# Kernel tuning notes

Hardware: AMD Instinct MI355X
Metric: run time of the kernel (lower is better)

The kernel has to match this reference:

```python
import jax, jax.numpy as jnp
import numpy as np

V, H, P, L, O = 47, 1024, 4, 3, 47
B, T = 256, 128


def setup_inputs() -> dict:
    key = jax.random.key(0)
    ks = jax.random.split(key, 10)
    s = 1.0 / np.sqrt(H)
    b_ih = jnp.zeros((L, 4 * H), jnp.float32).at[:, H:2 * H].set(1.0)  # forget-gate bias = 1
    return {
        "x": jax.random.randint(ks[0], (B, T), 0, V),
        "properties": jax.random.normal(ks[1], (B, P), jnp.float32),
        "emb": jax.random.normal(ks[2], (V, H), jnp.float32) * s,
        "W_dec": jax.random.normal(ks[3], (O, H), jnp.float32) * s,
        "b_dec": jnp.zeros((O,), jnp.float32),
        "W_ih0": jax.random.normal(ks[4], (4 * H, H + P), jnp.float32) * s,
        "W_ih_rest": jax.random.normal(ks[5], (L - 1, 4 * H, H), jnp.float32) * s,
        "W_hh": jax.random.normal(ks[6], (L, 4 * H, H), jnp.float32) * s,
        "b_ih": b_ih,
        "b_hh": jnp.zeros((L, 4 * H), jnp.float32),
    }


def _lstm_step(x_in, h, c, W_ih, W_hh, b_ih, b_hh):
    # x_in: [B, in_dim]; h, c: [B, H]; gate order i,f,g,o (PyTorch)
    gates = x_in @ W_ih.T + h @ W_hh.T + b_ih + b_hh  # [B, 4H]
    i, f, g, o = jnp.split(gates, 4, axis=-1)
    c_new = jax.nn.sigmoid(f) * c + jax.nn.sigmoid(i) * jnp.tanh(g)
    h_new = jax.nn.sigmoid(o) * jnp.tanh(c_new)
    return h_new, c_new


def reference(x, properties, emb, W_dec, b_dec, W_ih0, W_ih_rest, W_hh, b_ih, b_hh):
    bsz, max_length = x.shape
    h0 = jnp.zeros((L, bsz, H), emb.dtype)
    c0 = jnp.zeros((L, bsz, H), emb.dtype)
    inp0 = emb[jnp.zeros((bsz,), jnp.int32)]  # initial token id 0 -> [B, H]

    def step(carry, _):
        h, c, inp = carry
        x_in = jnp.concatenate([inp, properties], axis=-1)  # [B, H+P]
        hs, cs = [], []
        for l in range(L):
            W_ih_l = W_ih0 if l == 0 else W_ih_rest[l - 1]
            h_l, c_l = _lstm_step(x_in, h[l], c[l], W_ih_l, W_hh[l], b_ih[l], b_hh[l])
            hs.append(h_l); cs.append(c_l)
            x_in = h_l
        logits = x_in @ W_dec.T + b_dec  # [B, O]
        nxt = jnp.argmax(logits, axis=-1)  # greedy decode
        new_carry = (jnp.stack(hs), jnp.stack(cs), emb[nxt])
        return new_carry, logits

    (h, c, _), logits_seq = jax.lax.scan(step, (h0, c0, inp0), None, length=max_length)
    outputs = jnp.transpose(logits_seq, (1, 0, 2))  # [B, T, O]
    return outputs, h, c
```

## Files before the change

kernel.cpp:

```cpp
#include <hip/hip_runtime.h>
#include <hip/hip_bf16.h>
#include <cstdint>
#include <cstddef>


#define BB 256
#define TT 128
#define OO 47

typedef __attribute__((ext_vector_type(8))) _Float16 f16x8;
typedef __attribute__((ext_vector_type(4))) float f32x4;

#define CBUF_B   0u
#define HF32_B   3145728u
#define BCOMB_B  9437184u
#define EHI_B    9486336u
#define ELO_B    10027008u
#define HS_B     10567680u
#define W_B      16859136u
#define WS_NEEDED 118046720u

#define BARRIER() asm volatile("s_barrier" ::: "memory")
#define WAITV(n)  asm volatile("s_waitcnt vmcnt(" #n ")" ::: "memory")
#define WAITLGKM0() asm volatile("s_waitcnt lgkmcnt(0)" ::: "memory")

__device__ __forceinline__ float fsig(float x) {
  return 1.0f / (1.0f + exp2f(-1.4426950408889634f * x));
}
__device__ __forceinline__ float ftanhf(float x) {
  float e = exp2f(2.8853900817779268f * x);
  return 1.0f - 2.0f / (e + 1.0f);
}
__device__ __forceinline__ unsigned short f16b(_Float16 h) {
  union { _Float16 f; unsigned short u; } c; c.f = h; return c.u;
}
__device__ __forceinline__ void gld16(const void* g, void* l) {
  __builtin_amdgcn_global_load_lds(
      (const __attribute__((address_space(1))) unsigned int*)g,
      (__attribute__((address_space(3))) unsigned int*)l, 16, 0, 0);
}
__device__ __forceinline__ size_t slab_addr(int grp, int NCH, int k, int r) {
  return ((size_t)grp * NCH + (k >> 5)) * 512 + ((k >> 4) & 1) * 256 +
         ((k >> 3) & 1) * 128 + r * 8 + (k & 7);
}

__global__ void k_zero(float* p, int n) {
  int i = blockIdx.x * blockDim.x + threadIdx.x;
  int stride = gridDim.x * blockDim.x;
  for (; i < n; i += stride) p[i] = 0.0f;
}

__global__ void k_binit(float* bc, const float* __restrict__ bih,
                        const float* __restrict__ bhh) {
  int i = blockIdx.x * blockDim.x + threadIdx.x;
  if (i < 12288) bc[i] = bih[i] + bhh[i];
}

__global__ void k_prepw(const float* __restrict__ src, unsigned short* dhi,
                        unsigned short* dlo, int K, int NCH) {
  const int nrow = blockIdx.x;
  const int ngrp = nrow >> 4, rr = nrow & 15;
  const float* s = src + (size_t)nrow * K;
  for (int k = threadIdx.x; k < NCH * 32; k += blockDim.x) {
    float val = (k < K) ? s[k] : 0.0f;
    _Float16 h16 = (_Float16)val;
    _Float16 l16 = (_Float16)((val - (float)h16) * 2048.0f);
    size_t a = slab_addr(ngrp, NCH, k, rr);
    dhi[a] = f16b(h16);
    dlo[a] = f16b(l16);
  }
}

__global__ void k_einit(unsigned short* ehi, unsigned short* elo,
                        const float* __restrict__ emb,
                        const float* __restrict__ props) {
  const int b = blockIdx.x;
  for (int j = threadIdx.x; j < 1056; j += blockDim.x) {
    float val = (j < 1024) ? emb[j] : (j < 1028 ? props[b * 4 + (j - 1024)] : 0.0f);
    _Float16 h16 = (_Float16)val;
    _Float16 l16 = (_Float16)((val - (float)h16) * 2048.0f);
    size_t a = slab_addr(b >> 4, 33, j, b & 15);
    ehi[a] = f16b(h16);
    elo[a] = f16b(l16);
  }
}

__global__ __launch_bounds__(512, 4) void k_layer(
    const char* __restrict__ xhi, const char* __restrict__ xlo, int NCHX,
    const char* __restrict__ hhi, const char* __restrict__ hlo,
    const char* __restrict__ wxhi, const char* __restrict__ wxlo,
    const char* __restrict__ whhi, const char* __restrict__ whlo,
    const float* __restrict__ bcomb, float* __restrict__ cbuf,
    float* __restrict__ hdstf, unsigned short* __restrict__ hshi,
    unsigned short* __restrict__ hslo) {
  __shared__ char LBUF[65536];
  const int tid = threadIdx.x;
  const int lane = tid & 63, wid = tid >> 6;
  const int sw = ((blockIdx.x & 7) << 5) + (blockIdx.x >> 3);
  const int mt = sw & 3, nt = sw >> 2;
  const int m0 = mt << 6, h0c = nt << 4;
  const int nst = (NCHX > 32) ? NCHX : 32;

  const int sIsB = wid >> 2, sHalfW = (wid >> 1) & 1, sPrec = wid & 1;
  const int sNch = sHalfW ? 32 : NCHX;
  const char* sbase[4];
  {
    const char* t0;
    if (!sIsB) t0 = sHalfW ? (sPrec ? hlo : hhi) : (sPrec ? xlo : xhi);
    else       t0 = sHalfW ? (sPrec ? whlo : whhi) : (sPrec ? wxlo : wxhi);
#pragma unroll
    for (int i = 0; i < 4; ++i) {
      int grp = sIsB ? (i * 64 + nt) : (mt * 4 + i);
      sbase[i] = t0 + (size_t)grp * sNch * 1024 + (size_t)lane * 16;
    }
  }
  const int ldsoff0 = (sIsB << 14) + (sHalfW << 13) + (sPrec << 12);
  auto stage = [&](int s, int bufbase) {
    char* ldst = LBUF + bufbase + ldsoff0;
    const size_t so = (size_t)s * 1024;
#pragma unroll
    for (int i = 0; i < 4; ++i) gld16(sbase[i] + so, ldst + i * 1024);
  };

  const int wHalf = wid >> 2, q = wid & 3;
  const int mb = (q >> 1) << 1, nbb = (q & 1) << 1;
  const int waveNst = wHalf ? 32 : NCHX;

  f32x4 accH[4], accL[4];
#pragma unroll
  for (int i = 0; i < 4; ++i) {
    accH[i] = f32x4{0.f, 0.f, 0.f, 0.f};
    accL[i] = f32x4{0.f, 0.f, 0.f, 0.f};
  }

  stage(0, 0);
  stage(1, 32768);

  for (int s = 0; s < nst; ++s) {
    const int bufb = (s & 1) << 15;
    if (s + 1 < sNch) { WAITV(4); }
    else              { WAITV(0); }
    BARRIER();

    if (s < waveNst) {
      const char* A0 = LBUF + bufb + (wHalf << 13);
      const char* B0 = LBUF + bufb + 16384 + (wHalf << 13);
      f16x8 ah[2], al[2], bh[2], bl[2];
#pragma unroll
      for (int r = 0; r < 2; ++r) {
        ah[r] = *(const f16x8*)(A0 + ((mb + r) << 10) + (lane << 4));
        al[r] = *(const f16x8*)(A0 + 4096 + ((mb + r) << 10) + (lane << 4));
      }
#pragma unroll
      for (int c = 0; c < 2; ++c) {
        bh[c] = *(const f16x8*)(B0 + ((nbb + c) << 10) + (lane << 4));
        bl[c] = *(const f16x8*)(B0 + 4096 + ((nbb + c) << 10) + (lane << 4));
      }
      __builtin_amdgcn_s_setprio(1);
#pragma unroll
      for (int r = 0; r < 2; ++r)
#pragma unroll
        for (int c = 0; c < 2; ++c) {
          int ix = r * 2 + c;
          accH[ix] = __builtin_amdgcn_mfma_f32_16x16x32_f16(ah[r], bh[c], accH[ix], 0, 0, 0);
          accL[ix] = __builtin_amdgcn_mfma_f32_16x16x32_f16(al[r], bh[c], accL[ix], 0, 0, 0);
          accL[ix] = __builtin_amdgcn_mfma_f32_16x16x32_f16(ah[r], bl[c], accL[ix], 0, 0, 0);
        }
      __builtin_amdgcn_s_setprio(0);
    }

    WAITLGKM0();
    BARRIER();
    if (s + 2 < sNch) stage(s + 2, bufb);
  }

  BARRIER();
  float* GH = (float*)LBUF;
  float* GL = GH + 64 * 68;
  const int mrow0 = ((q >> 1) << 5) + ((lane >> 4) << 2);
  const int ncol0 = ((q & 1) << 5) + (lane & 15);
  if (wHalf == 0) {
#pragma unroll
    for (int r = 0; r < 2; ++r)
#pragma unroll
      for (int c = 0; c < 2; ++c) {
        f32x4 aH = accH[r * 2 + c], aL = accL[r * 2 + c];
        int mr = mrow0 + r * 16, nc = ncol0 + c * 16;
#pragma unroll
        for (int i = 0; i < 4; ++i) {
          GH[(mr + i) * 68 + nc] = aH[i];
          GL[(mr + i) * 68 + nc] = aL[i];
        }
      }
  }
  __syncthreads();
  if (wHalf == 1) {
#pragma unroll
    for (int r = 0; r < 2; ++r)
#pragma unroll
      for (int c = 0; c < 2; ++c) {
        f32x4 aH = accH[r * 2 + c], aL = accL[r * 2 + c];
        int mr = mrow0 + r * 16, nc = ncol0 + c * 16;
#pragma unroll
        for (int i = 0; i < 4; ++i) {
          GH[(mr + i) * 68 + nc] += aH[i];
          GL[(mr + i) * 68 + nc] += aL[i];
        }
      }
  }
  __syncthreads();

  const float LSC = 1.0f / 2048.0f;
#pragma unroll
  for (int e = 0; e < 2; ++e) {
    int ci = tid * 2 + e;
    int bl_ = ci >> 4, hh = ci & 15;
    int b = m0 + bl_, hcol = h0c + hh;
    float xi = GH[bl_ * 68 + hh]      + GL[bl_ * 68 + hh]      * LSC + bcomb[hcol];
    float xf = GH[bl_ * 68 + 16 + hh] + GL[bl_ * 68 + 16 + hh] * LSC + bcomb[1024 + hcol];
    float xg = GH[bl_ * 68 + 32 + hh] + GL[bl_ * 68 + 32 + hh] * LSC + bcomb[2048 + hcol];
    float xo = GH[bl_ * 68 + 48 + hh] + GL[bl_ * 68 + 48 + hh] * LSC + bcomb[3072 + hcol];
    size_t cidx = (size_t)b * 1024 + hcol;
    float cn = fsig(xf) * cbuf[cidx] + fsig(xi) * ftanhf(xg);
    float hn = fsig(xo) * ftanhf(cn);
    cbuf[cidx] = cn;
    hdstf[cidx] = hn;
    _Float16 h16 = (_Float16)hn;
    _Float16 l16 = (_Float16)((hn - (float)h16) * 2048.0f);
    size_t sa = slab_addr(b >> 4, 32, hcol, b & 15);
    hshi[sa] = f16b(h16);
    hslo[sa] = f16b(l16);
  }
}

__global__ __launch_bounds__(256) void k_decode(
    const float* __restrict__ h2, const float* __restrict__ Wdec,
    const float* __restrict__ bdec, const float* __restrict__ emb,
    float* __restrict__ out, unsigned short* __restrict__ ehi,
    unsigned short* __restrict__ elo, int t) {
  __shared__ float P[4][64];
  __shared__ int tokS;
  const int b = blockIdx.x;
  const int w = threadIdx.x >> 6, lane = threadIdx.x & 63;
  const float* hrow = h2 + (size_t)b * 1024 + w * 256;
  float part = 0.f;
  if (lane < OO) {
    const float* wrow = Wdec + (size_t)lane * 1024 + w * 256;
    float p0 = 0.f, p1 = 0.f, p2 = 0.f, p3 = 0.f;
    for (int k = 0; k < 256; k += 16) {
      float4 w0 = *(const float4*)(wrow + k);      float4 h0v = *(const float4*)(hrow + k);
      float4 w1 = *(const float4*)(wrow + k + 4);  float4 h1v = *(const float4*)(hrow + k + 4);
      float4 w2 = *(const float4*)(wrow + k + 8);  float4 h2v = *(const float4*)(hrow + k + 8);
      float4 w3 = *(const float4*)(wrow + k + 12); float4 h3v = *(const float4*)(hrow + k + 12);
      p0 += w0.x * h0v.x + w0.y * h0v.y + w0.z * h0v.z + w0.w * h0v.w;
      p1 += w1.x * h1v.x + w1.y * h1v.y + w1.z * h1v.z + w1.w * h1v.w;
      p2 += w2.x * h2v.x + w2.y * h2v.y + w2.z * h2v.z + w2.w * h2v.w;
      p3 += w3.x * h3v.x + w3.y * h3v.y + w3.z * h3v.z + w3.w * h3v.w;
    }
    part = (p0 + p1) + (p2 + p3);
  }
  P[w][lane] = part;
  __syncthreads();
  if (w == 0) {
    float logit = -3.0e38f;
    if (lane < OO)
      logit = P[0][lane] + P[1][lane] + P[2][lane] + P[3][lane] + bdec[lane];
    float vv = logit;
    int idx = (lane < OO) ? lane : 1000;
#pragma unroll
    for (int m = 1; m < 64; m <<= 1) {
      float v2 = __shfl_xor(vv, m, 64);
      int i2 = __shfl_xor(idx, m, 64);
      if (v2 > vv || (v2 == vv && i2 < idx)) { vv = v2; idx = i2; }
    }
    if (lane < OO) out[(size_t)b * (TT * OO) + t * OO + lane] = logit;
    if (lane == 0) tokS = idx;
  }
  __syncthreads();
  if (t < TT - 1) {
    const float* erow = emb + (size_t)tokS * 1024;
    float4 ev = ((const float4*)erow)[threadIdx.x];
    float vals[4] = {ev.x, ev.y, ev.z, ev.w};
#pragma unroll
    for (int r = 0; r < 4; ++r) {
      int j = threadIdx.x * 4 + r;
      _Float16 h16 = (_Float16)vals[r];
      _Float16 l16 = (_Float16)((vals[r] - (float)h16) * 2048.0f);
      size_t a = slab_addr(b >> 4, 33, j, b & 15);
      ehi[a] = f16b(h16);
      elo[a] = f16b(l16);
    }
  }
}

__global__ void k_final(const float* __restrict__ hf, const float* __restrict__ cb,
                        float* __restrict__ out) {
  int i = blockIdx.x * blockDim.x + threadIdx.x;
  int stride = gridDim.x * blockDim.x;
  const int HBASE = BB * TT * OO;
  for (; i < 2 * 786432; i += stride) {
    if (i < 786432) {
      int l = i >> 18, r = i & 262143;
      out[HBASE + i] = hf[(size_t)(l * 2 + 0) * 262144 + r];
    } else {
      int j = i - 786432;
      out[HBASE + 786432 + j] = cb[j];
    }
  }
}

#define O_EBUF  0
#define O_HPB   270336
#define O_CBUF  1843200
#define O_BCOMB 2629632
#define O_WSN   2641920
#define O_HP(l, p) (O_HPB + ((l) * 2 + (p)) * 262144)

__global__ void k_initO(float* ws, const float* __restrict__ props,
                        const float* __restrict__ emb,
                        const float* __restrict__ bih,
                        const float* __restrict__ bhh) {
  int i = blockIdx.x * blockDim.x + threadIdx.x;
  if (i < 270336) {
    int b = i / 1056, j = i % 1056;
    float v = 0.0f;
    if (j < 1024) v = emb[j];
    else if (j < 1028) v = props[b * 4 + (j - 1024)];
    ws[O_EBUF + i] = v;
  } else if (i < 270336 + 12288) {
    int j = i - 270336;
    ws[O_BCOMB + j] = bih[j] + bhh[j];
  }
}

__global__ __launch_bounds__(512, 2) void k_layerO(
    const float* __restrict__ xsrc, int xs, int Kx, int nst0,
    const float* __restrict__ hsrc,
    const float* __restrict__ Wx, int wxs,
    const float* __restrict__ Wh,
    const float* __restrict__ bcomb, float* __restrict__ cbuf,
    float* __restrict__ hdst) {
  __shared__ char LBUF[65536];
  const int tid = threadIdx.x;
  const int lane = tid & 63, wid = tid >> 6;
  const int sw = ((blockIdx.x & 7) << 5) + (blockIdx.x >> 3);
  const int mt = sw & 3, nt = sw >> 2;
  const int m0 = mt << 6, h0c = nt << 4;
  const int nstMax = (nst0 > 32) ? nst0 : 32;
  const int tile = tid >> 7;
  const int tt = tid & 127;
  const int srow = tt >> 1;
  const int kseg = (tt & 1) << 4;
  const int isB = tile >> 1, sHalf = tile & 1;
  const int myNst = sHalf ? 32 : nst0;
  const float* grow;
  int KactB = 0x7fffffff;
  if (!isB) {
    grow = sHalf ? (hsrc + (size_t)(m0 + srow) * 1024)
                 : (xsrc + (size_t)(m0 + srow) * xs);
  } else {
    int nrow = ((srow >> 4) << 10) + h0c + (srow & 15);
    grow = sHalf ? (Wh + (size_t)nrow * 1024) : (Wx + (size_t)nrow * wxs);
    KactB = sHalf ? 1024 : Kx;
  }
  const int wbase = ((srow >> 4) << 10) + ((tt & 1) << 9) + ((srow & 15) << 4);
  const int ssec = (isB << 14) + (sHalf << 13);
  const int wHalf = wid >> 2, q = wid & 3;
  const int mb = (q >> 1) << 1, nbb = (q & 1) << 1;
  const int waveNst = wHalf ? 32 : nst0;
  const int secAr = (wHalf << 13);
  const int secBr = 16384 + (wHalf << 13);
  f32x4 accH[4], accL[4];
#pragma unroll
  for (int i = 0; i < 4; ++i) {
    accH[i] = f32x4{0.f, 0.f, 0.f, 0.f};
    accL[i] = f32x4{0.f, 0.f, 0.f, 0.f};
  }
  float4 v[4];
  auto load_regs = [&](int s) {
    const int kl = (s << 5) + kseg;
    const float4* p = (const float4*)(grow + kl);
#pragma unroll
    for (int qq = 0; qq < 4; ++qq) {
      int kk = kl + qq * 4;
      if (kk < KactB) v[qq] = p[qq];
      else v[qq] = float4{0.f, 0.f, 0.f, 0.f};
    }
  };
  auto cvt_write = [&](int buf) {
    char* base = LBUF + buf * 32768 + ssec + wbase;
#pragma unroll
    for (int g = 0; g < 2; ++g) {
      float fs[8] = {v[2*g].x, v[2*g].y, v[2*g].z, v[2*g].w,
                     v[2*g+1].x, v[2*g+1].y, v[2*g+1].z, v[2*g+1].w};
      f16x8 hvv, lvv;
#pragma unroll
      for (int j = 0; j < 8; ++j) {
        _Float16 h16 = (_Float16)fs[j];
        lvv[j] = (_Float16)((fs[j] - (float)h16) * 2048.0f);
        hvv[j] = h16;
      }
      *(f16x8*)(base + g * 256) = hvv;
      *(f16x8*)(base + g * 256 + 4096) = lvv;
    }
  };
  load_regs(0);
  cvt_write(0);
  __syncthreads();
  for (int s = 0; s < nstMax; ++s) {
    const int cur = s & 1, nxt = cur ^ 1;
    const bool doStage = (s + 1 < myNst);
    if (doStage) load_regs(s + 1);
    if (s < waveNst) {
      const char* A0 = LBUF + cur * 32768 + secAr;
      const char* B0 = LBUF + cur * 32768 + secBr;
      f16x8 ah[2], al[2], bh[2], bl[2];
#pragma unroll
      for (int r = 0; r < 2; ++r) {
        ah[r] = *(const f16x8*)(A0 + ((mb + r) << 10) + (lane << 4));
        al[r] = *(const f16x8*)(A0 + 4096 + ((mb + r) << 10) + (lane << 4));
      }
#pragma unroll
      for (int c = 0; c < 2; ++c) {
        bh[c] = *(const f16x8*)(B0 + ((nbb + c) << 10) + (lane << 4));
        bl[c] = *(const f16x8*)(B0 + 4096 + ((nbb + c) << 10) + (lane << 4));
      }
#pragma unroll
      for (int r = 0; r < 2; ++r)
#pragma unroll
        for (int c = 0; c < 2; ++c) {
          int ix = r * 2 + c;
          accH[ix] = __builtin_amdgcn_mfma_f32_16x16x32_f16(ah[r], bh[c], accH[ix], 0, 0, 0);
          accL[ix] = __builtin_amdgcn_mfma_f32_16x16x32_f16(al[r], bh[c], accL[ix], 0, 0, 0);
          accL[ix] = __builtin_amdgcn_mfma_f32_16x16x32_f16(ah[r], bl[c], accL[ix], 0, 0, 0);
        }
    }
    if (doStage) cvt_write(nxt);
    __syncthreads();
  }
  float* GH = (float*)LBUF;
  float* GL = GH + 64 * 68;
  const int mrow0 = ((q >> 1) << 5) + ((lane >> 4) << 2);
  const int ncol0 = ((q & 1) << 5) + (lane & 15);
  if (wHalf == 0) {
#pragma unroll
    for (int r = 0; r < 2; ++r)
#pragma unroll
      for (int c = 0; c < 2; ++c) {
        f32x4 aHh = accH[r * 2 + c], aLl = accL[r * 2 + c];
        int mr = mrow0 + r * 16, nc = ncol0 + c * 16;
#pragma unroll
        for (int i = 0; i < 4; ++i) { GH[(mr + i) * 68 + nc] = aHh[i]; GL[(mr + i) * 68 + nc] = aLl[i]; }
      }
  }
  __syncthreads();
  if (wHalf == 1) {
#pragma unroll
    for (int r = 0; r < 2; ++r)
#pragma unroll
      for (int c = 0; c < 2; ++c) {
        f32x4 aHh = accH[r * 2 + c], aLl = accL[r * 2 + c];
        int mr = mrow0 + r * 16, nc = ncol0 + c * 16;
#pragma unroll
        for (int i = 0; i < 4; ++i) { GH[(mr + i) * 68 + nc] += aHh[i]; GL[(mr + i) * 68 + nc] += aLl[i]; }
      }
  }
  __syncthreads();
  const float LSC = 1.0f / 2048.0f;
#pragma unroll
  for (int e = 0; e < 2; ++e) {
    int ci = tid * 2 + e;
    int bl_ = ci >> 4, hh = ci & 15;
    int b = m0 + bl_, hcol = h0c + hh;
    float xi = GH[bl_ * 68 + hh]      + GL[bl_ * 68 + hh]      * LSC + bcomb[hcol];
    float xf = GH[bl_ * 68 + 16 + hh] + GL[bl_ * 68 + 16 + hh] * LSC + bcomb[1024 + hcol];
    float xg = GH[bl_ * 68 + 32 + hh] + GL[bl_ * 68 + 32 + hh] * LSC + bcomb[2048 + hcol];
    float xo = GH[bl_ * 68 + 48 + hh] + GL[bl_ * 68 + 48 + hh] * LSC + bcomb[3072 + hcol];
    size_t cidx = (size_t)b * 1024 + hcol;
    float cn = fsig(xf) * cbuf[cidx] + fsig(xi) * ftanhf(xg);
    float hn = fsig(xo) * ftanhf(cn);
    cbuf[cidx] = cn;
    hdst[cidx] = hn;
  }
}

__global__ __launch_bounds__(64) void k_decodeO(
    const float* __restrict__ h2, const float* __restrict__ Wdec,
    const float* __restrict__ bdec, const float* __restrict__ emb,
    float* __restrict__ out, float* __restrict__ ebuf, int t) {
  const int b = blockIdx.x, lane = threadIdx.x;
  const float* hrow = h2 + (size_t)b * 1024;
  float logit = 0.f;
  if (lane < OO) {
    const float* wrow = Wdec + (size_t)lane * 1024;
    float p0 = 0.f, p1 = 0.f, p2 = 0.f, p3 = 0.f;
    for (int k = 0; k < 1024; k += 16) {
      float4 w0 = *(const float4*)(wrow + k);      float4 h0v = *(const float4*)(hrow + k);
      float4 w1 = *(const float4*)(wrow + k + 4);  float4 h1v = *(const float4*)(hrow + k + 4);
      float4 w2 = *(const float4*)(wrow + k + 8);  float4 h2v = *(const float4*)(hrow + k + 8);
      float4 w3 = *(const float4*)(wrow + k + 12); float4 h3v = *(const float4*)(hrow + k + 12);
      p0 += w0.x * h0v.x + w0.y * h0v.y + w0.z * h0v.z + w0.w * h0v.w;
      p1 += w1.x * h1v.x + w1.y * h1v.y + w1.z * h1v.z + w1.w * h1v.w;
      p2 += w2.x * h2v.x + w2.y * h2v.y + w2.z * h2v.z + w2.w * h2v.w;
      p3 += w3.x * h3v.x + w3.y * h3v.y + w3.z * h3v.z + w3.w * h3v.w;
    }
    logit = ((p0 + p1) + (p2 + p3)) + bdec[lane];
  }
  float vv = (lane < OO) ? logit : -3.0e38f;
  int idx = (lane < OO) ? lane : 1000;
#pragma unroll
  for (int m = 1; m < 64; m <<= 1) {
    float v2 = __shfl_xor(vv, m, 64);
    int i2 = __shfl_xor(idx, m, 64);
    if (v2 > vv || (v2 == vv && i2 < idx)) { vv = v2; idx = i2; }
  }
  if (lane < OO) out[(size_t)b * (TT * OO) + t * OO + lane] = logit;
  if (t < TT - 1) {
    const float* erow = emb + (size_t)idx * 1024;
#pragma unroll
    for (int i = 0; i < 16; ++i) {
      int h = i * 64 + lane;
      ebuf[(size_t)b * 1056 + h] = erow[h];
    }
  }
}

__global__ void k_finalO(const float* __restrict__ ws, float* __restrict__ out) {
  int i = blockIdx.x * blockDim.x + threadIdx.x;
  int stride = gridDim.x * blockDim.x;
  const int HBASE = BB * TT * OO;
  for (; i < 2 * 786432; i += stride) {
    if (i < 786432) {
      int l = i >> 18, r = i & 262143;
      out[HBASE + i] = ws[O_HP(l, 0) + r];
    } else {
      int j = i - 786432;
      out[HBASE + 786432 + j] = ws[O_CBUF + j];
    }
  }
}

extern "C" void kernel_launch(void* const* d_in, const int* in_sizes, int n_in,
                              void* d_out, int out_size, void* d_ws, size_t ws_size,
                              hipStream_t stream) {
  const float* props = (const float*)d_in[1];
  const float* emb   = (const float*)d_in[2];
  const float* Wdec  = (const float*)d_in[3];
  const float* bdec  = (const float*)d_in[4];
  const float* Wih0  = (const float*)d_in[5];
  const float* Wihr  = (const float*)d_in[6];
  const float* Whh   = (const float*)d_in[7];
  const float* bih   = (const float*)d_in[8];
  const float* bhh   = (const float*)d_in[9];
  float* out = (float*)d_out;

  if (ws_size >= (size_t)WS_NEEDED) {
    char* base = (char*)d_ws;
    float* cb = (float*)(base + CBUF_B);
    float* hf = (float*)(base + HF32_B);
    float* bc = (float*)(base + BCOMB_B);
    unsigned short* Ehi = (unsigned short*)(base + EHI_B);
    unsigned short* Elo = (unsigned short*)(base + ELO_B);
    auto HS = [&](int l, int p, int prec) {
      return (unsigned short*)(base + HS_B + (size_t)((l * 2 + p) * 2 + prec) * 524288u);
    };
    unsigned short* Wp[12];
    {
      size_t off = W_B;
      Wp[0] = (unsigned short*)(base + off); off += 8650752u;
      Wp[1] = (unsigned short*)(base + off); off += 8650752u;
      for (int i = 2; i < 12; ++i) { Wp[i] = (unsigned short*)(base + off); off += 8388608u; }
    }

    k_zero<<<2048, 256, 0, stream>>>((float*)base, 2359296);
    k_zero<<<2048, 256, 0, stream>>>((float*)(base + HS_B), 1572864);
    k_binit<<<48, 256, 0, stream>>>(bc, bih, bhh);
    k_einit<<<256, 256, 0, stream>>>(Ehi, Elo, emb, props);
    k_prepw<<<4096, 256, 0, stream>>>(Wih0, Wp[0], Wp[1], 1028, 33);
    k_prepw<<<4096, 256, 0, stream>>>(Whh,                           Wp[2], Wp[3], 1024, 32);
    k_prepw<<<4096, 256, 0, stream>>>(Wihr,                          Wp[4], Wp[5], 1024, 32);
    k_prepw<<<4096, 256, 0, stream>>>(Whh + (size_t)4096 * 1024,     Wp[6], Wp[7], 1024, 32);
    k_prepw<<<4096, 256, 0, stream>>>(Wihr + (size_t)4096 * 1024,    Wp[8], Wp[9], 1024, 32);
    k_prepw<<<4096, 256, 0, stream>>>(Whh + (size_t)2 * 4096 * 1024, Wp[10], Wp[11], 1024, 32);

    for (int t = 0; t < TT; ++t) {
      const int p = t & 1, pn = p ^ 1;
      k_layer<<<256, 512, 0, stream>>>(
          (const char*)Ehi, (const char*)Elo, 33,
          (const char*)HS(0, p, 0), (const char*)HS(0, p, 1),
          (const char*)Wp[0], (const char*)Wp[1],
          (const char*)Wp[2], (const char*)Wp[3],
          bc, cb, hf + (size_t)(0 * 2 + pn) * 262144,
          HS(0, pn, 0), HS(0, pn, 1));
      k_layer<<<256, 512, 0, stream>>>(
          (const char*)HS(0, pn, 0), (const char*)HS(0, pn, 1), 32,
          (const char*)HS(1, p, 0), (const char*)HS(1, p, 1),
          (const char*)Wp[4], (const char*)Wp[5],
          (const char*)Wp[6], (const char*)Wp[7],
          bc + 4096, cb + 262144, hf + (size_t)(1 * 2 + pn) * 262144,
          HS(1, pn, 0), HS(1, pn, 1));
      k_layer<<<256, 512, 0, stream>>>(
          (const char*)HS(1, pn, 0), (const char*)HS(1, pn, 1), 32,
          (const char*)HS(2, p, 0), (const char*)HS(2, p, 1),
          (const char*)Wp[8], (const char*)Wp[9],
          (const char*)Wp[10], (const char*)Wp[11],
          bc + 8192, cb + 524288, hf + (size_t)(2 * 2 + pn) * 262144,
          HS(2, pn, 0), HS(2, pn, 1));
      k_decode<<<256, 256, 0, stream>>>(hf + (size_t)(2 * 2 + pn) * 262144,
                                        Wdec, bdec, emb, out, Ehi, Elo, t);
    }
    k_final<<<2048, 256, 0, stream>>>(hf, cb, out);
  } else {
    float* ws = (float*)d_ws;
    float* E  = ws + O_EBUF;
    float* cb = ws + O_CBUF;
    float* bc = ws + O_BCOMB;
    k_zero<<<2048, 256, 0, stream>>>(ws, O_WSN);
    k_initO<<<1104, 256, 0, stream>>>(ws, props, emb, bih, bhh);
    for (int t = 0; t < TT; ++t) {
      const int p = t & 1;
      k_layerO<<<256, 512, 0, stream>>>(E, 1056, 1028, 33, ws + O_HP(0, p),
                                        Wih0, 1028, Whh, bc, cb, ws + O_HP(0, p ^ 1));
      k_layerO<<<256, 512, 0, stream>>>(ws + O_HP(0, p ^ 1), 1024, 1024, 32,
                                        ws + O_HP(1, p), Wihr, 1024,
                                        Whh + (size_t)4096 * 1024,
                                        bc + 4096, cb + 262144, ws + O_HP(1, p ^ 1));
      k_layerO<<<256, 512, 0, stream>>>(ws + O_HP(1, p ^ 1), 1024, 1024, 32,
                                        ws + O_HP(2, p),
                                        Wihr + (size_t)4096 * 1024, 1024,
                                        Whh + (size_t)2 * 4096 * 1024,
                                        bc + 8192, cb + 524288, ws + O_HP(2, p ^ 1));
      k_decodeO<<<256, 64, 0, stream>>>(ws + O_HP(2, p ^ 1), Wdec, bdec, emb, out, E, t);
    }
    k_finalO<<<2048, 256, 0, stream>>>(ws, out);
  }
}
```

Measured before the change: 10.33 ms.

## Fuse per-step layer and decode launches into one persistent kernel with grid barriers

Replaces the 512 per-timestep kernel launches (three layers plus decode, 128 steps) with a single persistent kernel of 256 blocks. Blocks synchronise through a hierarchical atomic grid barrier: a counter per group of eight, then a global generation counter. This removes launch overhead and the implicit inter-kernel gaps. The cost is spin-wait barrier latency and a requirement that all 256 blocks be co-resident, since otherwise the barrier deadlocks. Decode now spreads across 8 waves instead of 4.

```diff
diff --git a/kernel.cpp b/kernel.cpp
--- a/kernel.cpp
+++ b/kernel.cpp
@@ -18,7 +18,8 @@
 #define ELO_B    10027008u
 #define HS_B     10567680u
 #define W_B      16859136u
-#define WS_NEEDED 118046720u
+#define BAR_B    118046720u
+#define WS_NEEDED 118047360u
 
 #define BARRIER() asm volatile("s_barrier" ::: "memory")
 #define WAITV(n)  asm volatile("s_waitcnt vmcnt(" #n ")" ::: "memory")
@@ -51,9 +52,10 @@
 }
 
 __global__ void k_binit(float* bc, const float* __restrict__ bih,
-                        const float* __restrict__ bhh) {
+                        const float* __restrict__ bhh, unsigned* bar) {
   int i = blockIdx.x * blockDim.x + threadIdx.x;
   if (i < 12288) bc[i] = bih[i] + bhh[i];
+  if (i < 160) bar[i] = 0u;
 }
 
 __global__ void k_prepw(const float* __restrict__ src, unsigned short* dhi,
@@ -85,210 +87,277 @@
   }
 }
 
-__global__ __launch_bounds__(512, 4) void k_layer(
-    const char* __restrict__ xhi, const char* __restrict__ xlo, int NCHX,
-    const char* __restrict__ hhi, const char* __restrict__ hlo,
-    const char* __restrict__ wxhi, const char* __restrict__ wxlo,
-    const char* __restrict__ whhi, const char* __restrict__ whlo,
-    const float* __restrict__ bcomb, float* __restrict__ cbuf,
-    float* __restrict__ hdstf, unsigned short* __restrict__ hshi,
-    unsigned short* __restrict__ hslo) {
+__device__ __forceinline__ void gbar(unsigned* bar, int bid) {
+  __syncthreads();
+  if (threadIdx.x == 0) {
+    unsigned* gen  = bar + 144;
+    unsigned* gcnt = bar + 128;
+    unsigned* myg  = bar + ((bid & 7) << 4);
+    unsigned g = __hip_atomic_load(gen, __ATOMIC_RELAXED, __HIP_MEMORY_SCOPE_AGENT);
+    unsigned o = __hip_atomic_fetch_add(myg, 1u, __ATOMIC_ACQ_REL, __HIP_MEMORY_SCOPE_AGENT);
+    if (o == 31u) {
+      __hip_atomic_store(myg, 0u, __ATOMIC_RELAXED, __HIP_MEMORY_SCOPE_AGENT);
+      unsigned og = __hip_atomic_fetch_add(gcnt, 1u, __ATOMIC_ACQ_REL, __HIP_MEMORY_SCOPE_AGENT);
+      if (og == 7u) {
+        __hip_atomic_store(gcnt, 0u, __ATOMIC_RELAXED, __HIP_MEMORY_SCOPE_AGENT);
+        __hip_atomic_store(gen, g + 1u, __ATOMIC_RELEASE, __HIP_MEMORY_SCOPE_AGENT);
+      }
+    }
+    while (__hip_atomic_load(gen, __ATOMIC_RELAXED, __HIP_MEMORY_SCOPE_AGENT) == g) {
+      asm volatile("s_sleep 2");
+    }
+    (void)__hip_atomic_load(gen, __ATOMIC_ACQUIRE, __HIP_MEMORY_SCOPE_AGENT);
+  }
+  __syncthreads();
+  if ((threadIdx.x & 63) == 0)
+    (void)__hip_atomic_load(bar + 144, __ATOMIC_ACQUIRE, __HIP_MEMORY_SCOPE_AGENT);
+}
+
+__global__ __launch_bounds__(512, 4) void k_mega(
+    char* __restrict__ base, const float* __restrict__ Wdec,
+    const float* __restrict__ bdec, const float* __restrict__ emb,
+    float* __restrict__ out) {
   __shared__ char LBUF[65536];
   const int tid = threadIdx.x;
   const int lane = tid & 63, wid = tid >> 6;
-  const int sw = ((blockIdx.x & 7) << 5) + (blockIdx.x >> 3);
+  const int bid = blockIdx.x;
+  const int sw = ((bid & 7) << 5) + (bid >> 3);
   const int mt = sw & 3, nt = sw >> 2;
   const int m0 = mt << 6, h0c = nt << 4;
-  const int nst = (NCHX > 32) ? NCHX : 32;
+
+  unsigned* bar = (unsigned*)(base + BAR_B);
+  float* cbufA = (float*)(base + CBUF_B);
+  float* hfA   = (float*)(base + HF32_B);
+  float* bcA   = (float*)(base + BCOMB_B);
+
+  const unsigned wOff[12] = {
+    16859136u, 25509888u, 34160640u, 42549248u, 50937856u, 59326464u,
+    67715072u, 76103680u, 84492288u, 92880896u, 101269504u, 109658112u};
 
   const int sIsB = wid >> 2, sHalfW = (wid >> 1) & 1, sPrec = wid & 1;
-  const int sNch = sHalfW ? 32 : NCHX;
-  const char* sbase[4];
-  {
-    const char* t0;
-    if (!sIsB) t0 = sHalfW ? (sPrec ? hlo : hhi) : (sPrec ? xlo : xhi);
-    else       t0 = sHalfW ? (sPrec ? whlo : whhi) : (sPrec ? wxlo : wxhi);
-#pragma unroll
-    for (int i = 0; i < 4; ++i) {
-      int grp = sIsB ? (i * 64 + nt) : (mt * 4 + i);
-      sbase[i] = t0 + (size_t)grp * sNch * 1024 + (size_t)lane * 16;
-    }
-  }
   const int ldsoff0 = (sIsB << 14) + (sHalfW << 13) + (sPrec << 12);
-  auto stage = [&](int s, int bufbase) {
-    char* ldst = LBUF + bufbase + ldsoff0;
-    const size_t so = (size_t)s * 1024;
-#pragma unroll
-    for (int i = 0; i < 4; ++i) gld16(sbase[i] + so, ldst + i * 1024);
-  };
-
   const int wHalf = wid >> 2, q = wid & 3;
   const int mb = (q >> 1) << 1, nbb = (q & 1) << 1;
-  const int waveNst = wHalf ? 32 : NCHX;
-
-  f32x4 accH[4], accL[4];
-#pragma unroll
-  for (int i = 0; i < 4; ++i) {
-    accH[i] = f32x4{0.f, 0.f, 0.f, 0.f};
-    accL[i] = f32x4{0.f, 0.f, 0.f, 0.f};
-  }
-
-  stage(0, 0);
-  stage(1, 32768);
-
-  for (int s = 0; s < nst; ++s) {
-    const int bufb = (s & 1) << 15;
-    if (s + 1 < sNch) { WAITV(4); }
-    else              { WAITV(0); }
-    BARRIER();
-
-    if (s < waveNst) {
-      const char* A0 = LBUF + bufb + (wHalf << 13);
-      const char* B0 = LBUF + bufb + 16384 + (wHalf << 13);
-      f16x8 ah[2], al[2], bh[2], bl[2];
-#pragma unroll
-      for (int r = 0; r < 2; ++r) {
-        ah[r] = *(const f16x8*)(A0 + ((mb + r) << 10) + (lane << 4));
-        al[r] = *(const f16x8*)(A0 + 4096 + ((mb + r) << 10) + (lane << 4));
-      }
-#pragma unroll
-      for (int c = 0; c < 2; ++c) {
-        bh[c] = *(const f16x8*)(B0 + ((nbb + c) << 10) + (lane << 4));
-        bl[c] = *(const f16x8*)(B0 + 4096 + ((nbb + c) << 10) + (lane << 4));
-      }
-      __builtin_amdgcn_s_setprio(1);
-#pragma unroll
-      for (int r = 0; r < 2; ++r)
-#pragma unroll
-        for (int c = 0; c < 2; ++c) {
-          int ix = r * 2 + c;
-          accH[ix] = __builtin_amdgcn_mfma_f32_16x16x32_f16(ah[r], bh[c], accH[ix], 0, 0, 0);
-          accL[ix] = __builtin_amdgcn_mfma_f32_16x16x32_f16(al[r], bh[c], accL[ix], 0, 0, 0);
-          accL[ix] = __builtin_amdgcn_mfma_f32_16x16x32_f16(ah[r], bl[c], accL[ix], 0, 0, 0);
-        }
-      __builtin_amdgcn_s_setprio(0);
-    }
-
-    WAITLGKM0();
-    BARRIER();
-    if (s + 2 < sNch) stage(s + 2, bufb);
-  }
-
-  BARRIER();
-  float* GH = (float*)LBUF;
-  float* GL = GH + 64 * 68;
   const int mrow0 = ((q >> 1) << 5) + ((lane >> 4) << 2);
   const int ncol0 = ((q & 1) << 5) + (lane & 15);
-  if (wHalf == 0) {
-#pragma unroll
-    for (int r = 0; r < 2; ++r)
-#pragma unroll
-      for (int c = 0; c < 2; ++c) {
-        f32x4 aH = accH[r * 2 + c], aL = accL[r * 2 + c];
-        int mr = mrow0 + r * 16, nc = ncol0 + c * 16;
-#pragma unroll
-        for (int i = 0; i < 4; ++i) {
-          GH[(mr + i) * 68 + nc] = aH[i];
-          GL[(mr + i) * 68 + nc] = aL[i];
+  const float LSC = 1.0f / 2048.0f;
+
+  for (int t = 0; t < TT; ++t) {
+    const int p = t & 1, pn = p ^ 1;
+
+    for (int l = 0; l < 3; ++l) {
+      const char *xhi, *xlo;
+      int NCHX;
+      if (l == 0) { xhi = base + EHI_B; xlo = base + ELO_B; NCHX = 33; }
+      else {
+        xhi = base + HS_B + (size_t)(((l - 1) * 2 + pn) * 2 + 0) * 524288u;
+        xlo = base + HS_B + (size_t)(((l - 1) * 2 + pn) * 2 + 1) * 524288u;
+        NCHX = 32;
+      }
+      const char* hhi = base + HS_B + (size_t)((l * 2 + p) * 2 + 0) * 524288u;
+      const char* hlo = base + HS_B + (size_t)((l * 2 + p) * 2 + 1) * 524288u;
+      const int wbase4 = (l == 0) ? 0 : (l == 1 ? 4 : 8);
+      const char* wxhi = base + wOff[wbase4 + 0];
+      const char* wxlo = base + wOff[wbase4 + 1];
+      const char* whhi = base + wOff[wbase4 + 2];
+      const char* whlo = base + wOff[wbase4 + 3];
+      const float* bcomb = bcA + l * 4096;
+      float* cbuf  = cbufA + (size_t)l * 262144;
+      float* hdstf = hfA + (size_t)(l * 2 + pn) * 262144;
+      unsigned short* hshi = (unsigned short*)(base + HS_B + (size_t)((l * 2 + pn) * 2 + 0) * 524288u);
+      unsigned short* hslo = (unsigned short*)(base + HS_B + (size_t)((l * 2 + pn) * 2 + 1) * 524288u);
+
+      const int nst = (NCHX > 32) ? NCHX : 32;
+      const int sNch = sHalfW ? 32 : NCHX;
+      const int waveNst = wHalf ? 32 : NCHX;
+
+      const char* sb0;
+      {
+        const char* t0;
+        if (!sIsB) t0 = sHalfW ? (sPrec ? hlo : hhi) : (sPrec ? xlo : xhi);
+        else       t0 = sHalfW ? (sPrec ? whlo : whhi) : (sPrec ? wxlo : wxhi);
+        sb0 = t0 + (size_t)lane * 16;
+      }
+      const char* sb[4];
+#pragma unroll
+      for (int i = 0; i < 4; ++i) {
+        int grp = sIsB ? (i * 64 + nt) : (mt * 4 + i);
+        sb[i] = sb0 + (size_t)grp * sNch * 1024;
+      }
+      auto stage = [&](int s, int bufbase) {
+        char* ldst = LBUF + bufbase + ldsoff0;
+        const size_t so = (size_t)s * 1024;
+#pragma unroll
+        for (int i = 0; i < 4; ++i) gld16(sb[i] + so, ldst + i * 1024);
+      };
+
+      f32x4 accH[4], accL[4];
+#pragma unroll
+      for (int i = 0; i < 4; ++i) {
+        accH[i] = f32x4{0.f, 0.f, 0.f, 0.f};
+        accL[i] = f32x4{0.f, 0.f, 0.f, 0.f};
+      }
+
+      stage(0, 0);
+      stage(1, 32768);
+
+      for (int s = 0; s < nst; ++s) {
+        const int bufb = (s & 1) << 15;
+        if (s + 1 < sNch) { WAITV(4); }
+        else              { WAITV(0); }
+        BARRIER();
+
+        if (s < waveNst) {
+          const char* A0 = LBUF + bufb + (wHalf << 13);
+          const char* B0 = LBUF + bufb + 16384 + (wHalf << 13);
+          f16x8 ah[2], al[2], bh[2], bl[2];
+#pragma unroll
+          for (int r = 0; r < 2; ++r) {
+            ah[r] = *(const f16x8*)(A0 + ((mb + r) << 10) + (lane << 4));
+            al[r] = *(const f16x8*)(A0 + 4096 + ((mb + r) << 10) + (lane << 4));
+          }
+#pragma unroll
+          for (int c = 0; c < 2; ++c) {
+            bh[c] = *(const f16x8*)(B0 + ((nbb + c) << 10) + (lane << 4));
+            bl[c] = *(const f16x8*)(B0 + 4096 + ((nbb + c) << 10) + (lane << 4));
+          }
+          __builtin_amdgcn_s_setprio(1);
+#pragma unroll
+          for (int r = 0; r < 2; ++r)
+#pragma unroll
+            for (int c = 0; c < 2; ++c) {
+              int ix = r * 2 + c;
+              accH[ix] = __builtin_amdgcn_mfma_f32_16x16x32_f16(ah[r], bh[c], accH[ix], 0, 0, 0);
+              accL[ix] = __builtin_amdgcn_mfma_f32_16x16x32_f16(al[r], bh[c], accL[ix], 0, 0, 0);
+              accL[ix] = __builtin_amdgcn_mfma_f32_16x16x32_f16(ah[r], bl[c], accL[ix], 0, 0, 0);
+            }
+          __builtin_amdgcn_s_setprio(0);
         }
-      }
-  }
-  __syncthreads();
-  if (wHalf == 1) {
-#pragma unroll
-    for (int r = 0; r < 2; ++r)
-#pragma unroll
-      for (int c = 0; c < 2; ++c) {
-        f32x4 aH = accH[r * 2 + c], aL = accL[r * 2 + c];
-        int mr = mrow0 + r * 16, nc = ncol0 + c * 16;
-#pragma unroll
-        for (int i = 0; i < 4; ++i) {
-          GH[(mr + i) * 68 + nc] += aH[i];
-          GL[(mr + i) * 68 + nc] += aL[i];
+
+        WAITLGKM0();
+        BARRIER();
+        if (s + 2 < sNch) stage(s + 2, bufb);
+      }
+
+      BARRIER();
+      float* GH = (float*)LBUF;
+      float* GL = GH + 64 * 68;
+      if (wHalf == 0) {
+#pragma unroll
+        for (int r = 0; r < 2; ++r)
+#pragma unroll
+          for (int c = 0; c < 2; ++c) {
+            f32x4 aH = accH[r * 2 + c], aL = accL[r * 2 + c];
+            int mr = mrow0 + r * 16, nc = ncol0 + c * 16;
+#pragma unroll
+            for (int i = 0; i < 4; ++i) {
+              GH[(mr + i) * 68 + nc] = aH[i];
+              GL[(mr + i) * 68 + nc] = aL[i];
+            }
+          }
+      }
+      __syncthreads();
+      if (wHalf == 1) {
+#pragma unroll
+        for (int r = 0; r < 2; ++r)
+#pragma unroll
+          for (int c = 0; c < 2; ++c) {
+            f32x4 aH = accH[r * 2 + c], aL = accL[r * 2 + c];
+            int mr = mrow0 + r * 16, nc = ncol0 + c * 16;
+#pragma unroll
+            for (int i = 0; i < 4; ++i) {
+              GH[(mr + i) * 68 + nc] += aH[i];
+              GL[(mr + i) * 68 + nc] += aL[i];
+            }
+          }
+      }
+      __syncthreads();
+
+#pragma unroll
+      for (int e = 0; e < 2; ++e) {
+        int ci = tid * 2 + e;
+        int bl_ = ci >> 4, hh = ci & 15;
+        int b = m0 + bl_, hcol = h0c + hh;
+        float xi = GH[bl_ * 68 + hh]      + GL[bl_ * 68 + hh]      * LSC + bcomb[hcol];
+        float xf = GH[bl_ * 68 + 16 + hh] + GL[bl_ * 68 + 16 + hh] * LSC + bcomb[1024 + hcol];
+        float xg = GH[bl_ * 68 + 32 + hh] + GL[bl_ * 68 + 32 + hh] * LSC + bcomb[2048 + hcol];
+        float xo = GH[bl_ * 68 + 48 + hh] + GL[bl_ * 68 + 48 + hh] * LSC + bcomb[3072 + hcol];
+        size_t cidx = (size_t)b * 1024 + hcol;
+        float cn = fsig(xf) * cbuf[cidx] + fsig(xi) * ftanhf(xg);
+        float hn = fsig(xo) * ftanhf(cn);
+        cbuf[cidx] = cn;
+        hdstf[cidx] = hn;
+        _Float16 h16 = (_Float16)hn;
+        _Float16 l16 = (_Float16)((hn - (float)h16) * 2048.0f);
+        size_t sa = slab_addr(b >> 4, 32, hcol, b & 15);
+        hshi[sa] = f16b(h16);
+        hslo[sa] = f16b(l16);
+      }
+
+      gbar(bar, bid);
+    }
+
+    {
+      float* P = (float*)LBUF;
+      int* tokSp = (int*)(LBUF + 2048);
+      const float* h2 = hfA + (size_t)(4 + pn) * 262144;
+      const int b = bid;
+      const float* hrow = h2 + (size_t)b * 1024 + wid * 128;
+      float part = 0.f;
+      if (lane < OO) {
+        const float* wrow = Wdec + (size_t)lane * 1024 + wid * 128;
+        float p0 = 0.f, p1 = 0.f, p2 = 0.f, p3 = 0.f;
+        for (int k = 0; k < 128; k += 16) {
+          float4 w0 = *(const float4*)(wrow + k);      float4 h0v = *(const float4*)(hrow + k);
+          float4 w1 = *(const float4*)(wrow + k + 4);  float4 h1v = *(const float4*)(hrow + k + 4);
+          float4 w2 = *(const float4*)(wrow + k + 8);  float4 h2v = *(const float4*)(hrow + k + 8);
+          float4 w3 = *(const float4*)(wrow + k + 12); float4 h3v = *(const float4*)(hrow + k + 12);
+          p0 += w0.x * h0v.x + w0.y * h0v.y + w0.z * h0v.z + w0.w * h0v.w;
+          p1 += w1.x * h1v.x + w1.y * h1v.y + w1.z * h1v.z + w1.w * h1v.w;
+          p2 += w2.x * h2v.x + w2.y * h2v.y + w2.z * h2v.z + w2.w * h2v.w;
+          p3 += w3.x * h3v.x + w3.y * h3v.y + w3.z * h3v.z + w3.w * h3v.w;
         }
-      }
-  }
-  __syncthreads();
-
-  const float LSC = 1.0f / 2048.0f;
-#pragma unroll
-  for (int e = 0; e < 2; ++e) {
-    int ci = tid * 2 + e;
-    int bl_ = ci >> 4, hh = ci & 15;
-    int b = m0 + bl_, hcol = h0c + hh;
-    float xi = GH[bl_ * 68 + hh]      + GL[bl_ * 68 + hh]      * LSC + bcomb[hcol];
-    float xf = GH[bl_ * 68 + 16 + hh] + GL[bl_ * 68 + 16 + hh] * LSC + bcomb[1024 + hcol];
-    float xg = GH[bl_ * 68 + 32 + hh] + GL[bl_ * 68 + 32 + hh] * LSC + bcomb[2048 + hcol];
-    float xo = GH[bl_ * 68 + 48 + hh] + GL[bl_ * 68 + 48 + hh] * LSC + bcomb[3072 + hcol];
-    size_t cidx = (size_t)b * 1024 + hcol;
-    float cn = fsig(xf) * cbuf[cidx] + fsig(xi) * ftanhf(xg);
-    float hn = fsig(xo) * ftanhf(cn);
-    cbuf[cidx] = cn;
-    hdstf[cidx] = hn;
-    _Float16 h16 = (_Float16)hn;
-    _Float16 l16 = (_Float16)((hn - (float)h16) * 2048.0f);
-    size_t sa = slab_addr(b >> 4, 32, hcol, b & 15);
-    hshi[sa] = f16b(h16);
-    hslo[sa] = f16b(l16);
-  }
-}
-
-__global__ __launch_bounds__(256) void k_decode(
-    const float* __restrict__ h2, const float* __restrict__ Wdec,
-    const float* __restrict__ bdec, const float* __restrict__ emb,
-    float* __restrict__ out, unsigned short* __restrict__ ehi,
-    unsigned short* __restrict__ elo, int t) {
-  __shared__ float P[4][64];
-  __shared__ int tokS;
-  const int b = blockIdx.x;
-  const int w = threadIdx.x >> 6, lane = threadIdx.x & 63;
-  const float* hrow = h2 + (size_t)b * 1024 + w * 256;
-  float part = 0.f;
-  if (lane < OO) {
-    const float* wrow = Wdec + (size_t)lane * 1024 + w * 256;
-    float p0 = 0.f, p1 = 0.f, p2 = 0.f, p3 = 0.f;
-    for (int k = 0; k < 256; k += 16) {
-      float4 w0 = *(const float4*)(wrow + k);      float4 h0v = *(const float4*)(hrow + k);
-      float4 w1 = *(const float4*)(wrow + k + 4);  float4 h1v = *(const float4*)(hrow + k + 4);
-      float4 w2 = *(const float4*)(wrow + k + 8);  float4 h2v = *(const float4*)(hrow + k + 8);
-      float4 w3 = *(const float4*)(wrow + k + 12); float4 h3v = *(const float4*)(hrow + k + 12);
-      p0 += w0.x * h0v.x + w0.y * h0v.y + w0.z * h0v.z + w0.w * h0v.w;
-      p1 += w1.x * h1v.x + w1.y * h1v.y + w1.z * h1v.z + w1.w * h1v.w;
-      p2 += w2.x * h2v.x + w2.y * h2v.y + w2.z * h2v.z + w2.w * h2v.w;
-      p3 += w3.x * h3v.x + w3.y * h3v.y + w3.z * h3v.z + w3.w * h3v.w;
-    }
-    part = (p0 + p1) + (p2 + p3);
-  }
-  P[w][lane] = part;
-  __syncthreads();
-  if (w == 0) {
-    float logit = -3.0e38f;
-    if (lane < OO)
-      logit = P[0][lane] + P[1][lane] + P[2][lane] + P[3][lane] + bdec[lane];
-    float vv = logit;
-    int idx = (lane < OO) ? lane : 1000;
-#pragma unroll
-    for (int m = 1; m < 64; m <<= 1) {
-      float v2 = __shfl_xor(vv, m, 64);
-      int i2 = __shfl_xor(idx, m, 64);
-      if (v2 > vv || (v2 == vv && i2 < idx)) { vv = v2; idx = i2; }
-    }
-    if (lane < OO) out[(size_t)b * (TT * OO) + t * OO + lane] = logit;
-    if (lane == 0) tokS = idx;
-  }
-  __syncthreads();
-  if (t < TT - 1) {
-    const float* erow = emb + (size_t)tokS * 1024;
-    float4 ev = ((const float4*)erow)[threadIdx.x];
-    float vals[4] = {ev.x, ev.y, ev.z, ev.w};
-#pragma unroll
-    for (int r = 0; r < 4; ++r) {
-      int j = threadIdx.x * 4 + r;
-      _Float16 h16 = (_Float16)vals[r];
-      _Float16 l16 = (_Float16)((vals[r] - (float)h16) * 2048.0f);
-      size_t a = slab_addr(b >> 4, 33, j, b & 15);
-      ehi[a] = f16b(h16);
-      elo[a] = f16b(l16);
+        part = (p0 + p1) + (p2 + p3);
+      }
+      P[wid * 64 + lane] = part;
+      __syncthreads();
+      if (wid == 0) {
+        float logit = -3.0e38f;
+        if (lane < OO) {
+          logit = bdec[lane];
+#pragma unroll
+          for (int w = 0; w < 8; ++w) logit += P[w * 64 + lane];
+        }
+        float vv = logit;
+        int idx = (lane < OO) ? lane : 1000;
+#pragma unroll
+        for (int m = 1; m < 64; m <<= 1) {
+          float v2 = __shfl_xor(vv, m, 64);
+          int i2 = __shfl_xor(idx, m, 64);
+          if (v2 > vv || (v2 == vv && i2 < idx)) { vv = v2; idx = i2; }
+        }
+        if (lane < OO) out[(size_t)b * (TT * OO) + t * OO + lane] = logit;
+        if (lane == 0) tokSp[0] = idx;
+      }
+      __syncthreads();
+      if (t < TT - 1 && tid < 256) {
+        int tok = tokSp[0];
+        const float* erow = emb + (size_t)tok * 1024;
+        float4 ev = ((const float4*)erow)[tid];
+        float vals[4] = {ev.x, ev.y, ev.z, ev.w};
+        unsigned short* ehi = (unsigned short*)(base + EHI_B);
+        unsigned short* elo = (unsigned short*)(base + ELO_B);
+#pragma unroll
+        for (int r = 0; r < 4; ++r) {
+          int j = tid * 4 + r;
+          _Float16 h16 = (_Float16)vals[r];
+          _Float16 l16 = (_Float16)((vals[r] - (float)h16) * 2048.0f);
+          size_t a = slab_addr(b >> 4, 33, j, b & 15);
+          ehi[a] = f16b(h16);
+          elo[a] = f16b(l16);
+        }
+      }
+      gbar(bar, bid);
     }
   }
 }
@@ -561,9 +630,7 @@
     float* bc = (float*)(base + BCOMB_B);
     unsigned short* Ehi = (unsigned short*)(base + EHI_B);
     unsigned short* Elo = (unsigned short*)(base + ELO_B);
-    auto HS = [&](int l, int p, int prec) {
-      return (unsigned short*)(base + HS_B + (size_t)((l * 2 + p) * 2 + prec) * 524288u);
-    };
+    unsigned* bar = (unsigned*)(base + BAR_B);
     unsigned short* Wp[12];
     {
       size_t off = W_B;
@@ -574,7 +641,7 @@
 
     k_zero<<<2048, 256, 0, stream>>>((float*)base, 2359296);
     k_zero<<<2048, 256, 0, stream>>>((float*)(base + HS_B), 1572864);
-    k_binit<<<48, 256, 0, stream>>>(bc, bih, bhh);
+    k_binit<<<48, 256, 0, stream>>>(bc, bih, bhh, bar);
     k_einit<<<256, 256, 0, stream>>>(Ehi, Elo, emb, props);
     k_prepw<<<4096, 256, 0, stream>>>(Wih0, Wp[0], Wp[1], 1028, 33);
     k_prepw<<<4096, 256, 0, stream>>>(Whh,                           Wp[2], Wp[3], 1024, 32);
@@ -583,32 +650,8 @@
     k_prepw<<<4096, 256, 0, stream>>>(Wihr + (size_t)4096 * 1024,    Wp[8], Wp[9], 1024, 32);
     k_prepw<<<4096, 256, 0, stream>>>(Whh + (size_t)2 * 4096 * 1024, Wp[10], Wp[11], 1024, 32);
 
-    for (int t = 0; t < TT; ++t) {
-      const int p = t & 1, pn = p ^ 1;
-      k_layer<<<256, 512, 0, stream>>>(
-          (const char*)Ehi, (const char*)Elo, 33,
-          (const char*)HS(0, p, 0), (const char*)HS(0, p, 1),
-          (const char*)Wp[0], (const char*)Wp[1],
-          (const char*)Wp[2], (const char*)Wp[3],
-          bc, cb, hf + (size_t)(0 * 2 + pn) * 262144,
-          HS(0, pn, 0), HS(0, pn, 1));
-      k_layer<<<256, 512, 0, stream>>>(
-          (const char*)HS(0, pn, 0), (const char*)HS(0, pn, 1), 32,
-          (const char*)HS(1, p, 0), (const char*)HS(1, p, 1),
-          (const char*)Wp[4], (const char*)Wp[5],
-          (const char*)Wp[6], (const char*)Wp[7],
-          bc + 4096, cb + 262144, hf + (size_t)(1 * 2 + pn) * 262144,
-          HS(1, pn, 0), HS(1, pn, 1));
-      k_layer<<<256, 512, 0, stream>>>(
-          (const char*)HS(1, pn, 0), (const char*)HS(1, pn, 1), 32,
-          (const char*)HS(2, p, 0), (const char*)HS(2, p, 1),
-          (const char*)Wp[8], (const char*)Wp[9],
-          (const char*)Wp[10], (const char*)Wp[11],
-          bc + 8192, cb + 524288, hf + (size_t)(2 * 2 + pn) * 262144,
-          HS(2, pn, 0), HS(2, pn, 1));
-      k_decode<<<256, 256, 0, stream>>>(hf + (size_t)(2 * 2 + pn) * 262144,
-                                        Wdec, bdec, emb, out, Ehi, Elo, t);
-    }
+    k_mega<<<256, 512, 0, stream>>>(base, Wdec, bdec, emb, out);
+
     k_final<<<2048, 256, 0, stream>>>(hf, cb, out);
   } else {
     float* ws = (float*)d_ws;
```

After: 23.42 ms. 127% more time.
